# Kernel optimization log

Measured on AMD Instinct MI355X. Metric: run time of the kernel, lower is better.

Reference implementation:

```python
import jax, jax.numpy as jnp
import numpy as np

B, S, D = 8, 1024, 1024
H = 16
DK = D // H  # 64, dim_k == dim_v
F = 4096
EPS = 1e-5


def _layernorm(x, w, b):
    mu = jnp.mean(x, axis=-1, keepdims=True)
    var = jnp.mean((x - mu) ** 2, axis=-1, keepdims=True)
    return (x - mu) * jax.lax.rsqrt(var + EPS) * w + b


def setup_inputs() -> dict:
    key = jax.random.key(0)
    ks = jax.random.split(key, 12)
    init = lambda k, shape: (jax.random.normal(k, shape, dtype=jnp.float32) * 0.02)
    return {
        "src": jax.random.normal(ks[0], (B, S, D), dtype=jnp.float32),
        "mask": jnp.zeros((S, S), dtype=jnp.float32),
        # per-head projections, stacked over heads: [H, D, DK]
        "Wq": init(ks[1], (H, D, DK)), "bq": jnp.zeros((H, DK), jnp.float32),
        "Wk": init(ks[2], (H, D, DK)), "bk": jnp.zeros((H, DK), jnp.float32),
        "Wv": init(ks[3], (H, D, DK)), "bv": jnp.zeros((H, DK), jnp.float32),
        "Wo": init(ks[4], (H * DK, D)), "bo": jnp.zeros((D,), jnp.float32),
        "ln1_w": jnp.ones((D,), jnp.float32), "ln1_b": jnp.zeros((D,), jnp.float32),
        "W1": init(ks[5], (D, F)), "b1": jnp.zeros((F,), jnp.float32),
        "W2": init(ks[6], (F, D)), "b2": jnp.zeros((D,), jnp.float32),
        "ln2_w": jnp.ones((D,), jnp.float32), "ln2_b": jnp.zeros((D,), jnp.float32),
    }


def reference(src, mask, Wq, bq, Wk, bk, Wv, bv, Wo, bo,
              ln1_w, ln1_b, W1, b1, W2, b2, ln2_w, ln2_b):
    # per-head projections (vectorized over heads): [B, H, S, DK]
    q = jnp.einsum('bsd,hdk->bhsk', src, Wq) + bq[None, :, None, :]
    k = jnp.einsum('bsd,hdk->bhsk', src, Wk) + bk[None, :, None, :]
    v = jnp.einsum('bsd,hdk->bhsk', src, Wv) + bv[None, :, None, :]
    scale = float(DK) ** 0.5
    logits = jnp.einsum('bhsk,bhtk->bhst', q, k) / scale  # [B,H,S,S]
    logits = logits + mask * (-1e9)
    attn = jax.nn.softmax(logits, axis=-1)
    ctx = jnp.einsum('bhst,bhtv->bhsv', attn, v)  # [B,H,S,DK]
    # concat heads along feature dim (head-major order matches torch cat)
    ctx = jnp.transpose(ctx, (0, 2, 1, 3)).reshape(B, S, H * DK)
    attn_out = ctx @ Wo + bo
    x = _layernorm(src + attn_out, ln1_w, ln1_b)
    ffn = jax.nn.relu(x @ W1 + b1) @ W2 + b2
    return _layernorm(x + ffn, ln2_w, ln2_b)
```

## Files before the change

kernel.cpp:

```cpp
#include <hip/hip_runtime.h>

#define BB 8
#define SS 1024
#define DD 1024
#define HH 16
#define DK 64
#define FF 4096
#define MM (BB*SS)

typedef __attribute__((ext_vector_type(8))) short short8;
typedef __attribute__((ext_vector_type(4))) short short4v;
typedef __attribute__((ext_vector_type(4))) float floatx4;

__device__ inline short f2bf(float f) {
  union { float f; unsigned u; } v; v.f = f;
  unsigned r = (v.u + 0x7FFFu + ((v.u >> 16) & 1u)) >> 16;
  return (short)r;
}
__device__ inline float bf2f(unsigned short u) {
  union { unsigned u; float f; } v; v.u = ((unsigned)u) << 16;
  return v.f;
}

__device__ inline void gload_lds16(const void* g, void* l) {
  __builtin_amdgcn_global_load_lds(
      (const __attribute__((address_space(1))) void*)g,
      (__attribute__((address_space(3))) void*)l, 16, 0, 0);
}

__device__ void tr64(const float* __restrict__ s, unsigned short* __restrict__ d,
                     int R, int C, int r0, int c0, float (*ld)[68], int tid) {
  {
    int r = tid >> 2, c16 = (tid & 3) * 16;
#pragma unroll
    for (int i = 0; i < 4; ++i)
      *(float4*)(&ld[r][c16 + i * 4]) =
          *(const float4*)(s + (size_t)(r0 + r) * C + c0 + c16 + i * 4);
  }
  __syncthreads();
  int c = tid >> 2, r16 = (tid & 3) * 16;
  short8 o0, o1;
#pragma unroll
  for (int i = 0; i < 8; ++i) {
    o0[i] = f2bf(ld[r16 + i][c]);
    o1[i] = f2bf(ld[r16 + 8 + i][c]);
  }
  unsigned short* dp = d + (size_t)(c0 + c) * R + r0 + r16;
  *(short8*)(dp) = o0;
  *(short8*)(dp + 8) = o1;
}

__global__ __launch_bounds__(256) void prep_all(
    const float* __restrict__ src,
    const float* __restrict__ Wq, const float* __restrict__ Wk,
    const float* __restrict__ Wv,
    const float* __restrict__ bq, const float* __restrict__ bk,
    const float* __restrict__ bv, const float* __restrict__ Wo,
    unsigned short* __restrict__ srcb, unsigned short* __restrict__ wqkvT,
    float* __restrict__ bqkv, unsigned short* __restrict__ woT) {
  __shared__ float ld[64][68];
  const int bid = blockIdx.x, tid = threadIdx.x;
  if (bid < 4096) {
    int i8 = (bid * 256 + tid) * 8;
    float4 a = *(const float4*)(src + i8);
    float4 b = *(const float4*)(src + i8 + 4);
    short8 o;
    o[0] = f2bf(a.x); o[1] = f2bf(a.y); o[2] = f2bf(a.z); o[3] = f2bf(a.w);
    o[4] = f2bf(b.x); o[5] = f2bf(b.y); o[6] = f2bf(b.z); o[7] = f2bf(b.w);
    *(short8*)(srcb + i8) = o;
  } else if (bid < 4864) {
    int idx = bid - 4096;
    int d0 = (idx & 15) * 64, h = (idx >> 4) & 15, z = idx >> 8;
    const float* W = (z == 0 ? Wq : z == 1 ? Wk : Wv) + (size_t)h * DD * DK;
    {
      int r = tid >> 2, c16 = (tid & 3) * 16;
#pragma unroll
      for (int i = 0; i < 4; ++i)
        *(float4*)(&ld[r][c16 + i * 4]) =
            *(const float4*)(W + (size_t)(d0 + r) * DK + c16 + i * 4);
    }
    __syncthreads();
    int dv = tid >> 2, d16 = (tid & 3) * 16;
    short8 o0, o1;
#pragma unroll
    for (int i = 0; i < 8; ++i) {
      o0[i] = f2bf(ld[d16 + i][dv]);
      o1[i] = f2bf(ld[d16 + 8 + i][dv]);
    }
    unsigned short* dst = wqkvT + (size_t)(z * 1024 + h * 64 + dv) * DD + d0 + d16;
    *(short8*)(dst) = o0;
    *(short8*)(dst + 8) = o1;
  } else if (bid < 4876) {
    int n = (bid - 4864) * 256 + tid;
    int z = n >> 10;
    const float* s = (z == 0 ? bq : z == 1 ? bk : bv);
    bqkv[n] = s[n & 1023];
  } else {
    int idx = bid - 4876;
    tr64(Wo, woT, 1024, 1024, (idx & 15) * 64, (idx >> 4) * 64, ld, tid);
  }
}

__global__ __launch_bounds__(256) void prep2(
    const unsigned short* __restrict__ qkv, const float* __restrict__ mask,
    const float* __restrict__ W1, const float* __restrict__ W2,
    unsigned short* __restrict__ kbb, unsigned short* __restrict__ vtb,
    unsigned short* __restrict__ maskb, unsigned short* __restrict__ w1T,
    unsigned short* __restrict__ w2T) {
  __shared__ float ldf[64][68];
  const int bid = blockIdx.x, tid = threadIdx.x;
  if (bid < 2048) {
    const int t0 = (bid & 15) * 64, h = (bid >> 4) & 15, b = bid >> 8;
    int row = tid >> 2, c = (tid & 3) * 16;
    const unsigned short* s = qkv + (size_t)(b * SS + t0 + row) * 3072 + 1024 + h * 64 + c;
    unsigned short* d = kbb + ((size_t)((b * HH + h) * SS + t0 + row)) * 64 + c;
    *(short8*)(d) = *(const short8*)(s);
    *(short8*)(d + 8) = *(const short8*)(s + 8);
  } else if (bid < 4096) {
    __shared__ unsigned short ld[64][72];
    const int i = bid - 2048;
    const int t0 = (i & 15) * 64, h = (i >> 4) & 15, b = i >> 8;
    {
      int r = tid >> 2, c16 = (tid & 3) * 16;
      const unsigned short* s = qkv + (size_t)(b * SS + t0 + r) * 3072 + 2048 + h * 64 + c16;
      *(short8*)(&ld[r][c16]) = *(const short8*)(s);
      *(short8*)(&ld[r][c16 + 8]) = *(const short8*)(s + 8);
    }
    __syncthreads();
    int dv = tid >> 2, t16 = (tid & 3) * 16;
    short8 o0, o1;
#pragma unroll
    for (int j = 0; j < 8; ++j) {
      o0[j] = (short)ld[t16 + j][dv];
      o1[j] = (short)ld[t16 + 8 + j][dv];
    }
    unsigned short* d = vtb + ((size_t)(b * HH + h) * DK + dv) * SS + t0 + t16;
    *(short8*)(d) = o0;
    *(short8*)(d + 8) = o1;
  } else if (bid < 4608) {
    int i8 = ((bid - 4096) * 256 + tid) * 8;
    float4 a = *(const float4*)(mask + i8);
    float4 b = *(const float4*)(mask + i8 + 4);
    short8 o;
    o[0] = f2bf(a.x * -1e9f); o[1] = f2bf(a.y * -1e9f);
    o[2] = f2bf(a.z * -1e9f); o[3] = f2bf(a.w * -1e9f);
    o[4] = f2bf(b.x * -1e9f); o[5] = f2bf(b.y * -1e9f);
    o[6] = f2bf(b.z * -1e9f); o[7] = f2bf(b.w * -1e9f);
    *(short8*)(maskb + i8) = o;
  } else if (bid < 5632) {
    int i = bid - 4608;
    tr64(W1, w1T, 1024, 4096, (i & 15) * 64, (i >> 4) * 64, ldf, tid);
  } else {
    int i = bid - 5632;
    tr64(W2, w2T, 4096, 1024, (i & 63) * 64, (i >> 6) * 64, ldf, tid);
  }
}

#define BARR asm volatile("s_barrier" ::: "memory")

#define LOAD_A(mh_) { \
  _Pragma("unroll") for (int m_ = 0; m_ < 4; ++m_) { \
    const int row_ = wr * 128 + (mh_) * 64 + m_ * 16 + lm; \
    _Pragma("unroll") for (int ks_ = 0; ks_ < 2; ++ks_) \
      a[m_][ks_] = *(const short8*)(lA + (size_t)row_ * 64 + \
                     (size_t)((((ks_ * 4 + quad) ^ (lm & 7)) * 8))); \
  } }

#define LOAD_B(nh_) { \
  _Pragma("unroll") for (int n_ = 0; n_ < 2; ++n_) { \
    const int row_ = wc * 64 + (nh_) * 32 + n_ * 16 + lm; \
    _Pragma("unroll") for (int ks_ = 0; ks_ < 2; ++ks_) \
      bfr[nh_][n_][ks_] = *(const short8*)(lB + (size_t)row_ * 64 + \
                     (size_t)((((ks_ * 4 + quad) ^ (lm & 7)) * 8))); \
  } }

#define STAGE_A(kt_, mh_, db_) { \
  const unsigned short* g_ = A + (size_t)m0 * K + (size_t)(kt_) * 64; \
  unsigned short* lt_ = lds + (db_) * 32768; \
  _Pragma("unroll") for (int c_ = 0; c_ < 2; ++c_) { \
    const int row_ = c_ * 128 + (mh_) * 64; \
    gload_lds16(g_ + (size_t)(row_ + srow) * K + chs * 8, \
                lt_ + (size_t)(row_ + wave * 8) * 64); \
  } }

#define STAGE_B(kt_, nh_, db_) { \
  const unsigned short* g_ = Bt + (size_t)n0 * K + (size_t)(kt_) * 64; \
  unsigned short* lt_ = lds + (db_) * 32768 + 16384; \
  _Pragma("unroll") for (int c_ = 0; c_ < 2; ++c_) { \
    const int row_ = c_ * 128 + hi128 + (nh_) * 32; \
    gload_lds16(g_ + (size_t)(row_ + r32) * K + chs * 8, \
                lt_ + (size_t)(row_ + (wave & 3) * 8) * 64); \
  } }

#define MFMA_PH(mh_, nh_) { \
  asm volatile("s_waitcnt lgkmcnt(0)" ::: "memory"); \
  __builtin_amdgcn_s_setprio(1); \
  _Pragma("unroll") for (int m_ = 0; m_ < 4; ++m_) \
    _Pragma("unroll") for (int n_ = 0; n_ < 2; ++n_) { \
      acc[(mh_) * 4 + m_][(nh_) * 2 + n_] = __builtin_amdgcn_mfma_f32_16x16x32_bf16( \
          bfr[nh_][n_][0], a[m_][0], acc[(mh_) * 4 + m_][(nh_) * 2 + n_], 0, 0, 0); \
      acc[(mh_) * 4 + m_][(nh_) * 2 + n_] = __builtin_amdgcn_mfma_f32_16x16x32_bf16( \
          bfr[nh_][n_][1], a[m_][1], acc[(mh_) * 4 + m_][(nh_) * 2 + n_], 0, 0, 0); \
    } \
  __builtin_amdgcn_s_setprio(0); }

template <int RELU>
__global__ __launch_bounds__(512, 2) void gemm256(
    const unsigned short* __restrict__ A, const unsigned short* __restrict__ Bt,
    const float* __restrict__ bias, unsigned short* __restrict__ C,
    int M, int N, int K) {
  extern __shared__ unsigned short lds[];
  const int tid = threadIdx.x;
  const int wave = tid >> 6, lane = tid & 63;
  const int lm = lane & 15, quad = lane >> 4;
  const int wr = wave >> 2, wc = wave & 3;

  const int nwg = gridDim.x;
  const int cpx = nwg >> 3;
  const int id = (blockIdx.x & 7) * cpx + (blockIdx.x >> 3);
  const int nbx = N >> 8;
  const int bx = id % nbx, by = id / nbx;
  const int n0 = bx << 8, m0 = by << 8;

  const int NT = K >> 6;

  const int srow = tid >> 3;
  const int chs = (tid & 7) ^ (srow & 7);
  const int hi128 = (tid >= 256) ? 64 : 0;
  const int r32 = (tid >> 3) & 31;

  floatx4 acc[8][4] = {};
  short8 a[4][2], bfr[2][2][2];

  STAGE_A(0, 0, 0); STAGE_B(0, 0, 0);
  STAGE_A(0, 1, 0); STAGE_B(0, 1, 0);
  STAGE_A(1, 0, 1); STAGE_B(1, 0, 1);
  asm volatile("s_waitcnt vmcnt(4)" ::: "memory");
  BARR;

  for (int kt = 0; kt < NT; ++kt) {
    const int bb = kt & 1;
    const unsigned short* lA = lds + bb * 32768;
    const unsigned short* lB = lA + 16384;
    LOAD_A(0); LOAD_B(0);
    if (kt + 1 < NT) STAGE_A(kt + 1, 1, bb ^ 1);
    BARR; MFMA_PH(0, 0); BARR;
    LOAD_B(1);
    if (kt + 1 < NT) STAGE_B(kt + 1, 1, bb ^ 1);
    BARR; MFMA_PH(0, 1); BARR;
    LOAD_A(1);
    if (kt + 2 < NT) STAGE_A(kt + 2, 0, bb);
    BARR; MFMA_PH(1, 0); BARR;
    if (kt + 2 < NT) STAGE_B(kt + 2, 0, bb);
    BARR; MFMA_PH(1, 1);
    if (kt + 2 < NT) asm volatile("s_waitcnt vmcnt(4)" ::: "memory");
    else             asm volatile("s_waitcnt vmcnt(0)" ::: "memory");
    BARR;
  }

#pragma unroll
  for (int mi = 0; mi < 8; ++mi) {
    const int row = m0 + wr * 128 + mi * 16 + lm;
#pragma unroll
    for (int nj = 0; nj < 4; ++nj) {
      const int col = n0 + wc * 64 + nj * 16 + (quad << 2);
      const float4 bv = *(const float4*)(bias + col);
      float vv[4] = {acc[mi][nj][0] + bv.x, acc[mi][nj][1] + bv.y,
                     acc[mi][nj][2] + bv.z, acc[mi][nj][3] + bv.w};
      short4v o;
#pragma unroll
      for (int r = 0; r < 4; ++r) {
        float v = vv[r];
        if (RELU) v = fmaxf(v, 0.f);
        o[r] = f2bf(v);
      }
      *(short4v*)(C + (size_t)row * N + col) = o;
    }
  }
}

__global__ __launch_bounds__(512) void attention_flash(
    const unsigned short* __restrict__ qkv, const unsigned short* __restrict__ kb,
    const unsigned short* __restrict__ vt, const unsigned short* __restrict__ maskb,
    unsigned short* __restrict__ ctx) {
  const int flat = blockIdx.x;
  const int bh = (flat & 7) + 8 * (flat >> 6);
  const int qt = (flat >> 3) & 7;
  const int b = bh >> 4, h = bh & 15;
  const int s0 = qt * 128;
  const int tid = threadIdx.x;
  const int wave = tid >> 6, lane = tid & 63;
  const int lm = lane & 15, quad = lane >> 4;

  __shared__ __align__(16) unsigned short Ks[64 * 64];
  __shared__ __align__(16) unsigned short Vs[64 * 64];
  __shared__ __align__(16) unsigned short Ms[128 * 64];
  __shared__ __align__(16) unsigned short Ps[8][16 * 72];

  const unsigned short* qp = qkv + (size_t)(b * SS + s0 + wave * 16 + lm) * 3072 + h * 64;
  const short8 qa0 = *(const short8*)(qp + quad * 8);
  const short8 qa1 = *(const short8*)(qp + quad * 8 + 32);

  const unsigned short* kbase = kb + (size_t)bh * SS * DK;
  const unsigned short* vbase = vt + (size_t)bh * DK * SS;
  const unsigned short* mbase = maskb + (size_t)s0 * SS;

  const int sr = lane >> 3, sj = lane & 7;
  float m_run = -3e38f, l_run = 0.f;
  floatx4 O[4] = {};

  for (int it = 0; it < 16; ++it) {
    const int t0 = it * 64;
    __syncthreads();
    {
      int r = wave * 8 + sr;
      gload_lds16(kbase + (size_t)(t0 + r) * 64 + (size_t)(sj ^ (r & 7)) * 8,
                  (char*)Ks + wave * 1024);
      gload_lds16(vbase + (size_t)r * SS + t0 + (size_t)(sj ^ (r & 7)) * 8,
                  (char*)Vs + wave * 1024);
      int q1 = wave * 8 + sr;
      gload_lds16(mbase + (size_t)q1 * SS + t0 + (size_t)(sj ^ (q1 & 7)) * 8,
                  (char*)Ms + wave * 1024);
      int q2 = 64 + wave * 8 + sr;
      gload_lds16(mbase + (size_t)q2 * SS + t0 + (size_t)(sj ^ (q2 & 7)) * 8,
                  (char*)Ms + 8192 + wave * 1024);
    }
    __syncthreads();

    float p[16];
    float mt = -3e38f;
    const int qr = wave * 16 + lm;
#pragma unroll
    for (int ts = 0; ts < 4; ++ts) {
      int r = ts * 16 + lm;
      short8 kf0 = *(const short8*)&Ks[(r * 8 + (quad ^ (r & 7))) * 8];
      short8 kf1 = *(const short8*)&Ks[(r * 8 + ((quad + 4) ^ (r & 7))) * 8];
      floatx4 c = {0.f, 0.f, 0.f, 0.f};
      c = __builtin_amdgcn_mfma_f32_16x16x32_bf16(kf0, qa0, c, 0, 0, 0);
      c = __builtin_amdgcn_mfma_f32_16x16x32_bf16(kf1, qa1, c, 0, 0, 0);
      int mj = (ts * 2 + (quad >> 1)) ^ (qr & 7);
      short4v mv = *(const short4v*)&Ms[(qr * 8 + mj) * 8 + (quad & 1) * 4];
#pragma unroll
      for (int r2 = 0; r2 < 4; ++r2) {
        float sv = c[r2] * 0.125f + bf2f((unsigned short)mv[r2]);
        p[ts * 4 + r2] = sv;
        mt = fmaxf(mt, sv);
      }
    }
    mt = fmaxf(mt, __shfl_xor(mt, 16));
    mt = fmaxf(mt, __shfl_xor(mt, 32));
    float mnew = fmaxf(m_run, mt);
    float alpha = __expf(m_run - mnew);
    float psum = 0.f;
#pragma unroll
    for (int i = 0; i < 16; ++i) { p[i] = __expf(p[i] - mnew); psum += p[i]; }
    psum += __shfl_xor(psum, 16);
    psum += __shfl_xor(psum, 32);
    l_run = l_run * alpha + psum;
    m_run = mnew;
#pragma unroll
    for (int d = 0; d < 4; ++d)
#pragma unroll
      for (int r2 = 0; r2 < 4; ++r2) O[d][r2] *= alpha;

    unsigned short* pw = &Ps[wave][lm * 72];
#pragma unroll
    for (int ts = 0; ts < 4; ++ts) {
      short4v pv4;
#pragma unroll
      for (int r2 = 0; r2 < 4; ++r2) pv4[r2] = f2bf(p[ts * 4 + r2]);
      *(short4v*)(pw + ts * 16 + quad * 4) = pv4;
    }

#pragma unroll
    for (int ks = 0; ks < 2; ++ks) {
      short8 pf = *(const short8*)(pw + ks * 32 + quad * 8);
#pragma unroll
      for (int d = 0; d < 4; ++d) {
        int dv = d * 16 + lm;
        short8 vf = *(const short8*)&Vs[(dv * 8 + ((ks * 4 + quad) ^ (dv & 7))) * 8];
        O[d] = __builtin_amdgcn_mfma_f32_16x16x32_bf16(vf, pf, O[d], 0, 0, 0);
      }
    }
  }

  const float inv = 1.f / l_run;
  unsigned short* cp = ctx + (size_t)(b * SS + s0 + wave * 16 + lm) * DD + h * 64;
#pragma unroll
  for (int d = 0; d < 4; ++d) {
    short4v o;
#pragma unroll
    for (int r2 = 0; r2 < 4; ++r2) o[r2] = f2bf(O[d][r2] * inv);
    *(short4v*)(cp + d * 16 + quad * 4) = o;
  }
}

template <int A_BF16, int OUT_BF16>
__global__ __launch_bounds__(256) void residual_ln(
    const void* __restrict__ a_, const unsigned short* __restrict__ rr,
    const float* __restrict__ w, const float* __restrict__ bias,
    void* __restrict__ out_) {
  const int row = blockIdx.x;
  const int t = threadIdx.x;
  float x[4];
  if (A_BF16) {
    short4v va = *(const short4v*)((const unsigned short*)a_ + (size_t)row * DD + t * 4);
#pragma unroll
    for (int i = 0; i < 4; ++i) x[i] = bf2f((unsigned short)va[i]);
  } else {
    float4 va = *(const float4*)((const float*)a_ + (size_t)row * DD + t * 4);
    x[0] = va.x; x[1] = va.y; x[2] = va.z; x[3] = va.w;
  }
  {
    short4v vr = *(const short4v*)(rr + (size_t)row * DD + t * 4);
#pragma unroll
    for (int i = 0; i < 4; ++i) x[i] += bf2f((unsigned short)vr[i]);
  }
  float s = 0.f, ss = 0.f;
#pragma unroll
  for (int i = 0; i < 4; ++i) { s += x[i]; ss += x[i] * x[i]; }
#pragma unroll
  for (int o = 32; o > 0; o >>= 1) {
    s  += __shfl_down(s, o);
    ss += __shfl_down(ss, o);
  }
  __shared__ float2 sred[4];
  int wid = t >> 6;
  if ((t & 63) == 0) sred[wid] = make_float2(s, ss);
  __syncthreads();
  float st = 0.f, sst = 0.f;
#pragma unroll
  for (int i = 0; i < 4; ++i) { st += sred[i].x; sst += sred[i].y; }
  float mu  = st * (1.f / 1024.f);
  float var = sst * (1.f / 1024.f) - mu * mu;
  float rsq = rsqrtf(var + 1e-5f);
  float4 vw = *(const float4*)(w + t * 4);
  float4 vb = *(const float4*)(bias + t * 4);
  float o[4];
  o[0] = (x[0] - mu) * rsq * vw.x + vb.x;
  o[1] = (x[1] - mu) * rsq * vw.y + vb.y;
  o[2] = (x[2] - mu) * rsq * vw.z + vb.z;
  o[3] = (x[3] - mu) * rsq * vw.w + vb.w;
  if (OUT_BF16) {
    short4v ov;
#pragma unroll
    for (int i = 0; i < 4; ++i) ov[i] = f2bf(o[i]);
    *(short4v*)((unsigned short*)out_ + (size_t)row * DD + t * 4) = ov;
  } else {
    float4 ov = {o[0], o[1], o[2], o[3]};
    *(float4*)((float*)out_ + (size_t)row * DD + t * 4) = ov;
  }
}

extern "C" void kernel_launch(void* const* d_in, const int* in_sizes, int n_in,
                              void* d_out, int out_size, void* d_ws, size_t ws_size,
                              hipStream_t stream) {
  const float* src  = (const float*)d_in[0];
  const float* mask = (const float*)d_in[1];
  const float* Wq = (const float*)d_in[2];  const float* bq = (const float*)d_in[3];
  const float* Wk = (const float*)d_in[4];  const float* bk = (const float*)d_in[5];
  const float* Wv = (const float*)d_in[6];  const float* bv = (const float*)d_in[7];
  const float* Wo = (const float*)d_in[8];  const float* bo = (const float*)d_in[9];
  const float* ln1w = (const float*)d_in[10]; const float* ln1b = (const float*)d_in[11];
  const float* W1 = (const float*)d_in[12]; const float* b1 = (const float*)d_in[13];
  const float* W2 = (const float*)d_in[14]; const float* b2 = (const float*)d_in[15];
  const float* ln2w = (const float*)d_in[16]; const float* ln2b = (const float*)d_in[17];
  float* out = (float*)d_out;

  const size_t NEED = 125841408;
  if (ws_size < NEED) return;

  char* ws = (char*)d_ws;
  unsigned short* qkv   = (unsigned short*)(ws);
  unsigned short* vtb   = (unsigned short*)(ws + 50331648);
  unsigned short* kbb   = (unsigned short*)(ws + 67108864);
  unsigned short* ctxb  = (unsigned short*)(ws + 83886080);
  unsigned short* srcb  = (unsigned short*)(ws + 100663296);
  unsigned short* w1T   = (unsigned short*)(ws + 100663296);
  unsigned short* w2T   = (unsigned short*)(ws + 109051904);
  unsigned short* wqkvT = (unsigned short*)(ws + 117440512);
  unsigned short* maskb = (unsigned short*)(ws + 117440512);
  unsigned short* woT   = (unsigned short*)(ws + 123731968);
  float*          bqkv  = (float*)(ws + 125829120);
  unsigned short* h1       = qkv;
  unsigned short* attn_out = kbb;
  unsigned short* xb       = ctxb;
  unsigned short* ffn      = kbb;

  static bool lds_init = false;
  if (!lds_init) {
    auto* k0 = gemm256<0>;
    auto* k1 = gemm256<1>;
    hipFuncSetAttribute((const void*)k0, hipFuncAttributeMaxDynamicSharedMemorySize, 131072);
    hipFuncSetAttribute((const void*)k1, hipFuncAttributeMaxDynamicSharedMemorySize, 131072);
    lds_init = true;
  }

  prep_all<<<5132, 256, 0, stream>>>(src, Wq, Wk, Wv, bq, bk, bv, Wo,
                                     srcb, wqkvT, bqkv, woT);
  gemm256<0><<<(3072 / 256) * (MM / 256), 512, 131072, stream>>>(srcb, wqkvT, bqkv, qkv, MM, 3072, DD);
  prep2<<<6656, 256, 0, stream>>>(qkv, mask, W1, W2, kbb, vtb, maskb, w1T, w2T);
  attention_flash<<<1024, 512, 0, stream>>>(qkv, kbb, vtb, maskb, ctxb);
  gemm256<0><<<(DD / 256) * (MM / 256), 512, 131072, stream>>>(ctxb, woT, bo, attn_out, MM, DD, DD);
  residual_ln<0, 1><<<MM, 256, 0, stream>>>(src, attn_out, ln1w, ln1b, xb);
  gemm256<1><<<(FF / 256) * (MM / 256), 512, 131072, stream>>>(xb, w1T, b1, h1, MM, FF, DD);
  gemm256<0><<<(DD / 256) * (MM / 256), 512, 131072, stream>>>(h1, w2T, b2, ffn, MM, DD, FF);
  residual_ln<1, 0><<<MM, 256, 0, stream>>>(xb, ffn, ln2w, ln2b, out);
}
```

Measured before the change: 560.7 us.

## Restructure GEMM main loop into 2x-unrolled pipeline with deeper prefetch and fewer barriers

The 256x256 bf16 GEMM main loop is unrolled by two k-tiles with fixed LDS buffer pointers, and the global-to-LDS staging is rescheduled so the A half-tile is issued one phase earlier (vmcnt(6) instead of vmcnt(4)). Global base pointers are precomputed once outside the loop. The barrier before each MFMA phase is replaced by a combined barrier, lgkmcnt wait and sched_barrier, and a partial lgkmcnt hint is added. The goal is to reduce barrier count and address arithmetic and to hide load latency better, at the cost of more code size and the assumption that NT is even.

```diff
diff --git a/kernel.cpp b/kernel.cpp
--- a/kernel.cpp
+++ b/kernel.cpp
@@ -156,44 +156,46 @@
   }
 }
 
-#define BARR asm volatile("s_barrier" ::: "memory")
-
-#define LOAD_A(mh_) { \
+#define BARE __builtin_amdgcn_s_barrier()
+#define VM6  asm volatile("s_waitcnt vmcnt(6)" ::: "memory")
+#define VM0  asm volatile("s_waitcnt vmcnt(0)" ::: "memory")
+#define PH_HINT asm volatile("s_waitcnt lgkmcnt(8)" ::: "memory")
+#define PH_SYNC { \
+  __builtin_amdgcn_s_barrier(); \
+  asm volatile("s_waitcnt lgkmcnt(0)" ::: "memory"); \
+  __builtin_amdgcn_sched_barrier(0); }
+
+#define LOAD_A(lA_, mh_) { \
   _Pragma("unroll") for (int m_ = 0; m_ < 4; ++m_) { \
     const int row_ = wr * 128 + (mh_) * 64 + m_ * 16 + lm; \
     _Pragma("unroll") for (int ks_ = 0; ks_ < 2; ++ks_) \
-      a[m_][ks_] = *(const short8*)(lA + (size_t)row_ * 64 + \
-                     (size_t)((((ks_ * 4 + quad) ^ (lm & 7)) * 8))); \
+      a[m_][ks_] = *(const short8*)((lA_) + (size_t)row_ * 64 + \
+                     (size_t)(((ks_ * 4 + quad) ^ (lm & 7)) * 8)); \
   } }
 
-#define LOAD_B(nh_) { \
+#define LOAD_B(lB_, nh_) { \
   _Pragma("unroll") for (int n_ = 0; n_ < 2; ++n_) { \
     const int row_ = wc * 64 + (nh_) * 32 + n_ * 16 + lm; \
     _Pragma("unroll") for (int ks_ = 0; ks_ < 2; ++ks_) \
-      bfr[nh_][n_][ks_] = *(const short8*)(lB + (size_t)row_ * 64 + \
-                     (size_t)((((ks_ * 4 + quad) ^ (lm & 7)) * 8))); \
+      bfr[nh_][n_][ks_] = *(const short8*)((lB_) + 16384 + (size_t)row_ * 64 + \
+                     (size_t)(((ks_ * 4 + quad) ^ (lm & 7)) * 8)); \
   } }
 
-#define STAGE_A(kt_, mh_, db_) { \
-  const unsigned short* g_ = A + (size_t)m0 * K + (size_t)(kt_) * 64; \
-  unsigned short* lt_ = lds + (db_) * 32768; \
+#define STAGE_A(kt_, mh_, lb_) { \
   _Pragma("unroll") for (int c_ = 0; c_ < 2; ++c_) { \
     const int row_ = c_ * 128 + (mh_) * 64; \
-    gload_lds16(g_ + (size_t)(row_ + srow) * K + chs * 8, \
-                lt_ + (size_t)(row_ + wave * 8) * 64); \
+    gload_lds16(gA + (size_t)(kt_) * 64 + (size_t)row_ * K, \
+                (lb_) + (size_t)(row_ + wave * 8) * 64); \
   } }
 
-#define STAGE_B(kt_, nh_, db_) { \
-  const unsigned short* g_ = Bt + (size_t)n0 * K + (size_t)(kt_) * 64; \
-  unsigned short* lt_ = lds + (db_) * 32768 + 16384; \
+#define STAGE_B(kt_, nh_, lb_) { \
   _Pragma("unroll") for (int c_ = 0; c_ < 2; ++c_) { \
     const int row_ = c_ * 128 + hi128 + (nh_) * 32; \
-    gload_lds16(g_ + (size_t)(row_ + r32) * K + chs * 8, \
-                lt_ + (size_t)(row_ + (wave & 3) * 8) * 64); \
+    gload_lds16(gB + (size_t)(kt_) * 64 + (size_t)row_ * K, \
+                (lb_) + 16384 + (size_t)(row_ + (wave & 3) * 8) * 64); \
   } }
 
 #define MFMA_PH(mh_, nh_) { \
-  asm volatile("s_waitcnt lgkmcnt(0)" ::: "memory"); \
   __builtin_amdgcn_s_setprio(1); \
   _Pragma("unroll") for (int m_ = 0; m_ < 4; ++m_) \
     _Pragma("unroll") for (int n_ = 0; n_ < 2; ++n_) { \
@@ -204,12 +206,52 @@
     } \
   __builtin_amdgcn_s_setprio(0); }
 
+#define KITER(e_, ST_) { \
+   \
+  LOAD_A(buf0, 0); LOAD_B(buf0, 0); \
+  STAGE_B((e_) + 1, 1, buf1); \
+  PH_HINT; PH_SYNC; MFMA_PH(0, 0); BARE; \
+   \
+  LOAD_B(buf0, 1); \
+  if (ST_) STAGE_A((e_) + 2, 0, buf0); \
+  PH_SYNC; MFMA_PH(0, 1); BARE; \
+   \
+  LOAD_A(buf0, 1); \
+  if (ST_) STAGE_B((e_) + 2, 0, buf0); \
+  PH_SYNC; MFMA_PH(1, 0); BARE; \
+   \
+  if (ST_) STAGE_A((e_) + 2, 1, buf0); \
+  PH_SYNC; MFMA_PH(1, 1); \
+  if (ST_) { VM6; } else { VM0; } \
+  BARE; \
+   \
+  LOAD_A(buf1, 0); LOAD_B(buf1, 0); \
+  if (ST_) STAGE_B((e_) + 2, 1, buf0); \
+  PH_HINT; PH_SYNC; MFMA_PH(0, 0); BARE; \
+   \
+  LOAD_B(buf1, 1); \
+  if (ST_) STAGE_A((e_) + 3, 0, buf1); \
+  PH_SYNC; MFMA_PH(0, 1); BARE; \
+   \
+  LOAD_A(buf1, 1); \
+  if (ST_) STAGE_B((e_) + 3, 0, buf1); \
+  PH_SYNC; MFMA_PH(1, 0); BARE; \
+   \
+  if (ST_) { \
+    STAGE_A((e_) + 3, 1, buf1); \
+    PH_SYNC; MFMA_PH(1, 1); VM6; BARE; \
+  } else { \
+    PH_SYNC; MFMA_PH(1, 1); \
+  } }
+
 template <int RELU>
 __global__ __launch_bounds__(512, 2) void gemm256(
     const unsigned short* __restrict__ A, const unsigned short* __restrict__ Bt,
     const float* __restrict__ bias, unsigned short* __restrict__ C,
     int M, int N, int K) {
   extern __shared__ unsigned short lds[];
+  unsigned short* buf0 = lds;
+  unsigned short* buf1 = lds + 32768;
   const int tid = threadIdx.x;
   const int wave = tid >> 6, lane = tid & 63;
   const int lm = lane & 15, quad = lane >> 4;
@@ -228,35 +270,24 @@
   const int chs = (tid & 7) ^ (srow & 7);
   const int hi128 = (tid >= 256) ? 64 : 0;
   const int r32 = (tid >> 3) & 31;
+  const unsigned short* gA = A + (size_t)(m0 + srow) * K + chs * 8;
+  const unsigned short* gB = Bt + (size_t)(n0 + r32) * K + chs * 8;
 
   floatx4 acc[8][4] = {};
   short8 a[4][2], bfr[2][2][2];
 
-  STAGE_A(0, 0, 0); STAGE_B(0, 0, 0);
-  STAGE_A(0, 1, 0); STAGE_B(0, 1, 0);
-  STAGE_A(1, 0, 1); STAGE_B(1, 0, 1);
-  asm volatile("s_waitcnt vmcnt(4)" ::: "memory");
-  BARR;
-
-  for (int kt = 0; kt < NT; ++kt) {
-    const int bb = kt & 1;
-    const unsigned short* lA = lds + bb * 32768;
-    const unsigned short* lB = lA + 16384;
-    LOAD_A(0); LOAD_B(0);
-    if (kt + 1 < NT) STAGE_A(kt + 1, 1, bb ^ 1);
-    BARR; MFMA_PH(0, 0); BARR;
-    LOAD_B(1);
-    if (kt + 1 < NT) STAGE_B(kt + 1, 1, bb ^ 1);
-    BARR; MFMA_PH(0, 1); BARR;
-    LOAD_A(1);
-    if (kt + 2 < NT) STAGE_A(kt + 2, 0, bb);
-    BARR; MFMA_PH(1, 0); BARR;
-    if (kt + 2 < NT) STAGE_B(kt + 2, 0, bb);
-    BARR; MFMA_PH(1, 1);
-    if (kt + 2 < NT) asm volatile("s_waitcnt vmcnt(4)" ::: "memory");
-    else             asm volatile("s_waitcnt vmcnt(0)" ::: "memory");
-    BARR;
-  }
+  STAGE_A(0, 0, buf0); STAGE_B(0, 0, buf0);
+  STAGE_A(0, 1, buf0); STAGE_B(0, 1, buf0);
+  STAGE_A(1, 0, buf1); STAGE_B(1, 0, buf1);
+  STAGE_A(1, 1, buf1);
+  VM6;
+  BARE;
+
+  const int TT = NT >> 1;
+  for (int i = 0; i < TT - 1; ++i) {
+    KITER(2 * i, 1);
+  }
+  KITER(NT - 2, 0);
 
 #pragma unroll
   for (int mi = 0; mi < 8; ++mi) {
```

Result: faster. 545.9 us (-2.6%).
